# Performance work log

Measured on AMD Instinct MI355X. Metric: run time of the kernel, lower is better.

Reference implementation:

```python
import jax, jax.numpy as jnp
import numpy as np

PSI = 0.001  # convex-combination reconditioning strength
C, N, B = 4, 64, 2048


def _symmap(A, f, psi):
    # recondition via convex combination with identity, then apply f to the spectrum
    if psi > 0:
        A = (1.0 - psi) * A + psi * jnp.eye(A.shape[-1], dtype=A.dtype)
    L, Q = jnp.linalg.eigh(A)
    # Q diag(f(L)) Q^T
    return jnp.einsum('...ik,...k,...jk->...ij', Q, f(L), Q)


def setup_inputs() -> dict:
    key = jax.random.key(0)
    k1, k2 = jax.random.split(key)
    A = jax.random.normal(k1, (B, N, N), dtype=jnp.float32)
    inp = A @ A.swapaxes(-1, -2) / N + 0.1 * jnp.eye(N, dtype=jnp.float32)  # SPD [B,N,N]
    W = jax.random.normal(k2, (C, N, N), dtype=jnp.float32)
    weight = W @ W.swapaxes(-1, -2)  # module init: weight = W W^T, [C,N,N]
    return {'input': inp, 'weight': weight}


def reference(input, weight):
    # Omega^{-1/2} for each of the C tangency points
    ref_sri = _symmap(weight, lambda x: 1.0 / jnp.sqrt(x), PSI)  # [C,N,N]
    # congruence: Omega^{-1/2} Theta Omega^{-1/2}, broadcast over channels -> [B,C,N,N]
    cong = ref_sri @ input[..., None, :, :] @ ref_sri
    cong = 0.5 * (cong + cong.swapaxes(-1, -2))  # resymmetrize for eigh
    # matrix logarithm -> tangent-space vector field [B,C,N,N]
    return _symmap(cong, jnp.log, PSI)
```

## Files before the change

### kernel.cpp

```cpp
#include <hip/hip_runtime.h>
#include <math.h>

#define N 64
#define CSTR 68

typedef float f32x2 __attribute__((ext_vector_type(2)));

struct __align__(16) Smem {
    float mat[N * CSTR];
    float nbuf[2 * N];
    f32x2 obuf[2][N];
};

__device__ __forceinline__ float bperm(int byteaddr, float v) {
    return __int_as_float(__builtin_amdgcn_ds_bpermute(byteaddr, __float_as_int(v)));
}
__device__ __forceinline__ float rlane(float v, int k) {
    return __int_as_float(__builtin_amdgcn_readlane(__float_as_int(v), k));
}
__device__ __forceinline__ float dot4(float4 a, float4 b) {
    return fmaf(a.x, b.x, fmaf(a.y, b.y, fmaf(a.z, b.z, a.w * b.w)));
}

__device__ float jacobi_b128(float4 (&g)[8], int lane, int wid, Smem& S, int max_sweeps) {
    float4* ownc = (float4*)&S.mat[lane * CSTR + 32 * wid];
    float d = 0.f;
#pragma clang loop unroll(disable)
    for (int s = 0; s < max_sweeps; ++s) {
        float nh = 0.f;
#pragma unroll
        for (int i = 0; i < 8; ++i) nh += dot4(g[i], g[i]);
        S.nbuf[wid * N + lane] = nh;
        __syncthreads();
        d = S.nbuf[lane] + S.nbuf[N + lane];
        int anybad = 0, anybig = 0;
#pragma clang loop unroll(disable)
        for (int m = 1; m < N; ++m) {
            const float4* pc = (const float4*)&S.mat[(lane ^ m) * CSTR + 32 * wid];
            float4 t[8];
#pragma unroll
            for (int i = 0; i < 8; ++i) t[i] = pc[i];
            float op = 0.f;
#pragma unroll
            for (int i = 0; i < 8; ++i) op += dot4(g[i], t[i]);
            float doth = bperm((lane ^ m) << 2, d);
            int p = m & 1;
            ((float*)&S.obuf[p][lane])[wid] = op;
            __syncthreads();
            f32x2 ov = S.obuf[p][lane];
            float o = ov.x + ov.y;
            bool is_lo = lane < (lane ^ m);
            float dp = is_lo ? d : doth;
            float dq = is_lo ? doth : d;
            float oo = o * o, pq = dp * dq;
            int roundbad = __any(oo > 4e-10f * pq);
            anybad |= roundbad;
            anybig |= __any(oo > 1e-7f * pq);
            if (!roundbad) continue;
            bool skip = oo <= (1e-24f * pq);
            float osafe = skip ? 1.0f : o;
            float theta = (dq - dp) * 0.5f * __builtin_amdgcn_rcpf(osafe);
            float tt = -copysignf(
                __builtin_amdgcn_rcpf(fabsf(theta) + sqrtf(fmaf(theta, theta, 1.0f))),
                theta);
            float cc = rsqrtf(fmaf(tt, tt, 1.0f));
            float sv = tt * cc;
            cc = skip ? 1.0f : cc;
            sv = skip ? 0.0f : sv;
            float c2 = cc * cc, s2 = sv * sv, cso = 2.0f * cc * sv * o;
            d = is_lo ? fmaf(c2, dp, fmaf(s2, dq, cso))
                      : fmaf(s2, dp, fmaf(c2, dq, -cso));
            d = fmaxf(d, 1e-30f);
            float ss = is_lo ? sv : -sv;
#pragma unroll
            for (int i = 0; i < 8; ++i) {
                g[i].x = fmaf(ss, t[i].x, cc * g[i].x);
                g[i].y = fmaf(ss, t[i].y, cc * g[i].y);
                g[i].z = fmaf(ss, t[i].z, cc * g[i].z);
                g[i].w = fmaf(ss, t[i].w, cc * g[i].w);
            }
#pragma unroll
            for (int i = 0; i < 8; ++i) ownc[i] = g[i];
        }
        if (!__any(anybad) || !anybig) break;
    }
    float nh = 0.f;
#pragma unroll
    for (int i = 0; i < 8; ++i) nh += dot4(g[i], g[i]);
    S.nbuf[wid * N + lane] = nh;
    __syncthreads();
    d = S.nbuf[lane] + S.nbuf[N + lane];
    return d;
}

__device__ void recon_store(const float4 (&g)[8], float coef, int lane, int wid,
                            Smem& S, float* __restrict__ outp) {
    int row0 = wid * 32;
    float4 acc[8];
#pragma unroll
    for (int i = 0; i < 8; ++i) acc[i] = (float4){0.f, 0.f, 0.f, 0.f};
#pragma clang loop unroll(disable)
    for (int k = 0; k < N; ++k) {
        float wk = rlane(coef, k) * S.mat[k * CSTR + lane];
#pragma unroll
        for (int i = 0; i < 8; ++i) {
            acc[i].x = fmaf(rlane(g[i].x, k), wk, acc[i].x);
            acc[i].y = fmaf(rlane(g[i].y, k), wk, acc[i].y);
            acc[i].z = fmaf(rlane(g[i].z, k), wk, acc[i].z);
            acc[i].w = fmaf(rlane(g[i].w, k), wk, acc[i].w);
        }
    }
#pragma unroll
    for (int i = 0; i < 8; ++i) {
        outp[(row0 + 4 * i + 0) * N + lane] = acc[i].x;
        outp[(row0 + 4 * i + 1) * N + lane] = acc[i].y;
        outp[(row0 + 4 * i + 2) * N + lane] = acc[i].z;
        outp[(row0 + 4 * i + 3) * N + lane] = acc[i].w;
    }
}

__global__ __launch_bounds__(128, 4) void prep_R(const float* __restrict__ wgt,
                                                 float* __restrict__ Rws) {
    __shared__ Smem S;
    int c = blockIdx.x;
    int tid = threadIdx.x, wid = tid >> 6, lane = tid & 63;
    int row0 = wid * 32;
    const float* W = wgt + (size_t)c * (N * N);
    float4 g[8];
#pragma unroll
    for (int i = 0; i < 8; ++i) {
        float v[4];
#pragma unroll
        for (int q = 0; q < 4; ++q) {
            int rr = row0 + 4 * i + q;
            v[q] = 0.999f * W[rr * N + lane] + (rr == lane ? 0.001f : 0.f);
        }
        g[i] = (float4){v[0], v[1], v[2], v[3]};
    }
    float4* ownc = (float4*)&S.mat[lane * CSTR + row0];
#pragma unroll
    for (int i = 0; i < 8; ++i) ownc[i] = g[i];
    float d = jacobi_b128(g, lane, wid, S, 15);
    float coef = sqrtf(rsqrtf(d)) / d;
    recon_store(g, coef, lane, wid, S, Rws + (size_t)c * (N * N));
}

__global__ __launch_bounds__(128, 4) void tangent_log(const float* __restrict__ inp,
                                                      const float* __restrict__ Rws,
                                                      float* __restrict__ out) {
    __shared__ Smem S;
    int bid = blockIdx.x, b = bid >> 2, c = bid & 3;
    int tid = threadIdx.x, wid = tid >> 6, lane = tid & 63;
    int row0 = wid * 32;
    const float* Th = inp + (size_t)b * (N * N);
    const float* Rc = Rws + (size_t)c * (N * N);

    f32x2 r[32];
#pragma unroll
    for (int k = 0; k < 32; ++k) {
        r[k].x = Rc[(2 * k) * N + lane];
        r[k].y = Rc[(2 * k + 1) * N + lane];
    }
#pragma clang loop unroll(disable)
    for (int i = 0; i < 32; ++i) {
        const float4* __restrict__ row = (const float4*)(Th + (size_t)(row0 + i) * N);
        f32x2 a = {0.f, 0.f}, bacc = {0.f, 0.f};
#pragma unroll
        for (int q = 0; q < 16; q += 2) {
            float4 v0 = row[q], v1 = row[q + 1];
            a    = (f32x2){v0.x, v0.y} * r[2 * q]     + a;
            a    = (f32x2){v0.z, v0.w} * r[2 * q + 1] + a;
            bacc = (f32x2){v1.x, v1.y} * r[2 * q + 2] + bacc;
            bacc = (f32x2){v1.z, v1.w} * r[2 * q + 3] + bacc;
        }
        f32x2 sres = a + bacc;
        S.mat[lane * CSTR + row0 + i] = sres.x + sres.y;
    }
    __syncthreads();
    f32x2 ucol[32];
    {
        const f32x2* myc = (const f32x2*)&S.mat[lane * CSTR];
#pragma unroll
        for (int k = 0; k < 32; ++k) ucol[k] = myc[k];
    }
    __syncthreads();
#pragma clang loop unroll(disable)
    for (int i = 0; i < 32; ++i) {
        const float4* __restrict__ row = (const float4*)(Rc + (size_t)(row0 + i) * N);
        f32x2 a = {0.f, 0.f}, bacc = {0.f, 0.f};
#pragma unroll
        for (int q = 0; q < 16; q += 2) {
            float4 v0 = row[q], v1 = row[q + 1];
            a    = (f32x2){v0.x, v0.y} * ucol[2 * q]     + a;
            a    = (f32x2){v0.z, v0.w} * ucol[2 * q + 1] + a;
            bacc = (f32x2){v1.x, v1.y} * ucol[2 * q + 2] + bacc;
            bacc = (f32x2){v1.z, v1.w} * ucol[2 * q + 3] + bacc;
        }
        f32x2 sres = a + bacc;
        S.mat[lane * CSTR + row0 + i] = sres.x + sres.y;
    }
    __syncthreads();
    float4 g[8];
    {
        float4 own[8];
        const float4* oc = (const float4*)&S.mat[lane * CSTR + row0];
#pragma unroll
        for (int i = 0; i < 8; ++i) own[i] = oc[i];
        float tr[32];
#pragma unroll
        for (int i = 0; i < 32; ++i) tr[i] = S.mat[(row0 + i) * CSTR + lane];
        __syncthreads();
#pragma unroll
        for (int i = 0; i < 8; ++i) {
            float v[4];
#pragma unroll
            for (int q = 0; q < 4; ++q) {
                int rr = row0 + 4 * i + q;
                float ov = (q == 0) ? own[i].x : (q == 1) ? own[i].y : (q == 2) ? own[i].z : own[i].w;
                float sym = 0.5f * (ov + tr[4 * i + q]);
                v[q] = 0.999f * sym + (rr == lane ? 0.001f : 0.f);
            }
            g[i] = (float4){v[0], v[1], v[2], v[3]};
        }
        float4* wc = (float4*)&S.mat[lane * CSTR + row0];
#pragma unroll
        for (int i = 0; i < 8; ++i) wc[i] = g[i];
    }

    float d = jacobi_b128(g, lane, wid, S, 15);
    float coef = 0.5f * logf(d) / d;
    recon_store(g, coef, lane, wid, S, out + (size_t)bid * (N * N));
}

extern "C" void kernel_launch(void* const* d_in, const int* in_sizes, int n_in,
                              void* d_out, int out_size, void* d_ws, size_t ws_size,
                              hipStream_t stream) {
    const float* inp = (const float*)d_in[0];
    const float* wgt = (const float*)d_in[1];
    float* out = (float*)d_out;
    float* Rws = (float*)d_ws;

    int B = in_sizes[0] / (N * N);
    int C = in_sizes[1] / (N * N);

    hipLaunchKernelGGL(prep_R, dim3(C), dim3(128), 0, stream, wgt, Rws);
    hipLaunchKernelGGL(tangent_log, dim3(B * C), dim3(128), 0, stream, inp, Rws, out);
}
```

Baseline: 4.879 ms.

## Assign one matrix per wavefront to eliminate block barriers in Jacobi

Each 64x64 eigensolve now runs on a single wavefront instead of being split across two waves. This removes the __syncthreads and the LDS partial-dot exchange on every one of the 63 pair rotations per sweep. Each lane holds a full column of 64 floats and works with packed f32x2 FMAs. Two independent matrices share a 128-thread block, each with its own LDS tile. The cost is doubled per-lane register use (launch bounds drop to 2 blocks per CU) and half as many lanes working on each matrix.

```diff
diff --git a/kernel.cpp b/kernel.cpp
--- a/kernel.cpp
+++ b/kernel.cpp
@@ -6,49 +6,53 @@
 
 typedef float f32x2 __attribute__((ext_vector_type(2)));
 
-struct __align__(16) Smem {
-    float mat[N * CSTR];
-    float nbuf[2 * N];
-    f32x2 obuf[2][N];
-};
-
 __device__ __forceinline__ float bperm(int byteaddr, float v) {
     return __int_as_float(__builtin_amdgcn_ds_bpermute(byteaddr, __float_as_int(v)));
 }
 __device__ __forceinline__ float rlane(float v, int k) {
     return __int_as_float(__builtin_amdgcn_readlane(__float_as_int(v), k));
 }
-__device__ __forceinline__ float dot4(float4 a, float4 b) {
-    return fmaf(a.x, b.x, fmaf(a.y, b.y, fmaf(a.z, b.z, a.w * b.w)));
-}
-
-__device__ float jacobi_b128(float4 (&g)[8], int lane, int wid, Smem& S, int max_sweeps) {
-    float4* ownc = (float4*)&S.mat[lane * CSTR + 32 * wid];
+__device__ __forceinline__ f32x2 lo2(float4 v) { return (f32x2){v.x, v.y}; }
+__device__ __forceinline__ f32x2 hi2(float4 v) { return (f32x2){v.z, v.w}; }
+__device__ __forceinline__ float4 join4(f32x2 a, f32x2 b) { return (float4){a.x, a.y, b.x, b.y}; }
+__device__ __forceinline__ f32x2 pkfma(f32x2 a, f32x2 b, f32x2 c) {
+    return __builtin_elementwise_fma(a, b, c);
+}
+
+__device__ float jacobi_wave(float4 (&g)[16], int lane, float* __restrict__ mat,
+                             int max_sweeps) {
+    float4* __restrict__ ownc = (float4*)&mat[lane * CSTR];
     float d = 0.f;
 #pragma clang loop unroll(disable)
     for (int s = 0; s < max_sweeps; ++s) {
-        float nh = 0.f;
-#pragma unroll
-        for (int i = 0; i < 8; ++i) nh += dot4(g[i], g[i]);
-        S.nbuf[wid * N + lane] = nh;
-        __syncthreads();
-        d = S.nbuf[lane] + S.nbuf[N + lane];
+        {
+            f32x2 na = {0.f, 0.f}, nb = {0.f, 0.f};
+#pragma unroll
+            for (int i = 0; i < 16; ++i) {
+                na = pkfma(lo2(g[i]), lo2(g[i]), na);
+                nb = pkfma(hi2(g[i]), hi2(g[i]), nb);
+            }
+            f32x2 ns = na + nb;
+            d = ns.x + ns.y;
+        }
         int anybad = 0, anybig = 0;
 #pragma clang loop unroll(disable)
         for (int m = 1; m < N; ++m) {
-            const float4* pc = (const float4*)&S.mat[(lane ^ m) * CSTR + 32 * wid];
-            float4 t[8];
-#pragma unroll
-            for (int i = 0; i < 8; ++i) t[i] = pc[i];
-            float op = 0.f;
-#pragma unroll
-            for (int i = 0; i < 8; ++i) op += dot4(g[i], t[i]);
+            const float4* __restrict__ pc = (const float4*)&mat[(lane ^ m) * CSTR];
+            float4 t[16];
+#pragma unroll
+            for (int i = 0; i < 16; ++i) t[i] = pc[i];
+            f32x2 oa = {0.f, 0.f}, ob = {0.f, 0.f}, oc = {0.f, 0.f}, od = {0.f, 0.f};
+#pragma unroll
+            for (int i = 0; i < 8; ++i) {
+                oa = pkfma(lo2(g[2 * i]),     lo2(t[2 * i]),     oa);
+                ob = pkfma(hi2(g[2 * i]),     hi2(t[2 * i]),     ob);
+                oc = pkfma(lo2(g[2 * i + 1]), lo2(t[2 * i + 1]), oc);
+                od = pkfma(hi2(g[2 * i + 1]), hi2(t[2 * i + 1]), od);
+            }
+            f32x2 os = (oa + ob) + (oc + od);
+            float o = os.x + os.y;
             float doth = bperm((lane ^ m) << 2, d);
-            int p = m & 1;
-            ((float*)&S.obuf[p][lane])[wid] = op;
-            __syncthreads();
-            f32x2 ov = S.obuf[p][lane];
-            float o = ov.x + ov.y;
             bool is_lo = lane < (lane ^ m);
             float dp = is_lo ? d : doth;
             float dq = is_lo ? doth : d;
@@ -72,164 +76,153 @@
                       : fmaf(s2, dp, fmaf(c2, dq, -cso));
             d = fmaxf(d, 1e-30f);
             float ss = is_lo ? sv : -sv;
-#pragma unroll
-            for (int i = 0; i < 8; ++i) {
-                g[i].x = fmaf(ss, t[i].x, cc * g[i].x);
-                g[i].y = fmaf(ss, t[i].y, cc * g[i].y);
-                g[i].z = fmaf(ss, t[i].z, cc * g[i].z);
-                g[i].w = fmaf(ss, t[i].w, cc * g[i].w);
+            f32x2 cc2 = {cc, cc}, ss2 = {ss, ss};
+#pragma unroll
+            for (int i = 0; i < 16; ++i) {
+                f32x2 glo = pkfma(ss2, lo2(t[i]), lo2(g[i]) * cc2);
+                f32x2 ghi = pkfma(ss2, hi2(t[i]), hi2(g[i]) * cc2);
+                g[i] = join4(glo, ghi);
+                ownc[i] = g[i];
             }
-#pragma unroll
-            for (int i = 0; i < 8; ++i) ownc[i] = g[i];
-        }
-        if (!__any(anybad) || !anybig) break;
-    }
-    float nh = 0.f;
-#pragma unroll
-    for (int i = 0; i < 8; ++i) nh += dot4(g[i], g[i]);
-    S.nbuf[wid * N + lane] = nh;
-    __syncthreads();
-    d = S.nbuf[lane] + S.nbuf[N + lane];
-    return d;
-}
-
-__device__ void recon_store(const float4 (&g)[8], float coef, int lane, int wid,
-                            Smem& S, float* __restrict__ outp) {
-    int row0 = wid * 32;
-    float4 acc[8];
-#pragma unroll
-    for (int i = 0; i < 8; ++i) acc[i] = (float4){0.f, 0.f, 0.f, 0.f};
+        }
+        if (!anybad || !anybig) break;
+    }
+    f32x2 na = {0.f, 0.f}, nb = {0.f, 0.f};
+#pragma unroll
+    for (int i = 0; i < 16; ++i) {
+        na = pkfma(lo2(g[i]), lo2(g[i]), na);
+        nb = pkfma(hi2(g[i]), hi2(g[i]), nb);
+    }
+    f32x2 ns = na + nb;
+    return ns.x + ns.y;
+}
+
+__device__ void recon_store(const float4 (&g)[16], float coef, int lane,
+                            const float* __restrict__ mat, float* __restrict__ outp) {
+    f32x2 acc[32];
+#pragma unroll
+    for (int i = 0; i < 32; ++i) acc[i] = (f32x2){0.f, 0.f};
 #pragma clang loop unroll(disable)
     for (int k = 0; k < N; ++k) {
-        float wk = rlane(coef, k) * S.mat[k * CSTR + lane];
-#pragma unroll
-        for (int i = 0; i < 8; ++i) {
-            acc[i].x = fmaf(rlane(g[i].x, k), wk, acc[i].x);
-            acc[i].y = fmaf(rlane(g[i].y, k), wk, acc[i].y);
-            acc[i].z = fmaf(rlane(g[i].z, k), wk, acc[i].z);
-            acc[i].w = fmaf(rlane(g[i].w, k), wk, acc[i].w);
-        }
-    }
-#pragma unroll
-    for (int i = 0; i < 8; ++i) {
-        outp[(row0 + 4 * i + 0) * N + lane] = acc[i].x;
-        outp[(row0 + 4 * i + 1) * N + lane] = acc[i].y;
-        outp[(row0 + 4 * i + 2) * N + lane] = acc[i].z;
-        outp[(row0 + 4 * i + 3) * N + lane] = acc[i].w;
-    }
-}
-
-__global__ __launch_bounds__(128, 4) void prep_R(const float* __restrict__ wgt,
-                                                 float* __restrict__ Rws) {
-    __shared__ Smem S;
-    int c = blockIdx.x;
+        float wk = rlane(coef, k) * mat[k * CSTR + lane];
+        f32x2 wk2 = {wk, wk};
+#pragma unroll
+        for (int i = 0; i < 16; ++i) {
+            f32x2 b0 = {rlane(g[i].x, k), rlane(g[i].y, k)};
+            f32x2 b1 = {rlane(g[i].z, k), rlane(g[i].w, k)};
+            acc[2 * i]     = pkfma(b0, wk2, acc[2 * i]);
+            acc[2 * i + 1] = pkfma(b1, wk2, acc[2 * i + 1]);
+        }
+    }
+#pragma unroll
+    for (int i = 0; i < 32; ++i) {
+        outp[(size_t)(2 * i) * N + lane]     = acc[i].x;
+        outp[(size_t)(2 * i + 1) * N + lane] = acc[i].y;
+    }
+}
+
+__global__ __launch_bounds__(128, 2) void prep_R(const float* __restrict__ wgt,
+                                                 float* __restrict__ Rws, int C) {
+    __shared__ float S[2][N * CSTR];
     int tid = threadIdx.x, wid = tid >> 6, lane = tid & 63;
-    int row0 = wid * 32;
-    const float* W = wgt + (size_t)c * (N * N);
-    float4 g[8];
-#pragma unroll
-    for (int i = 0; i < 8; ++i) {
-        float v[4];
-#pragma unroll
-        for (int q = 0; q < 4; ++q) {
-            int rr = row0 + 4 * i + q;
-            v[q] = 0.999f * W[rr * N + lane] + (rr == lane ? 0.001f : 0.f);
-        }
-        g[i] = (float4){v[0], v[1], v[2], v[3]};
-    }
-    float4* ownc = (float4*)&S.mat[lane * CSTR + row0];
-#pragma unroll
-    for (int i = 0; i < 8; ++i) ownc[i] = g[i];
-    float d = jacobi_b128(g, lane, wid, S, 15);
+    int c = blockIdx.x * 2 + wid;
+    if (c >= C) return;
+    c = __builtin_amdgcn_readfirstlane(c);
+    const float* __restrict__ W = wgt + (size_t)c * (N * N);
+    float* __restrict__ mat = S[wid];
+    float4 g[16];
+#pragma unroll
+    for (int i = 0; i < 16; ++i) {
+        float v0 = 0.999f * W[(4 * i + 0) * N + lane] + ((4 * i + 0) == lane ? 0.001f : 0.f);
+        float v1 = 0.999f * W[(4 * i + 1) * N + lane] + ((4 * i + 1) == lane ? 0.001f : 0.f);
+        float v2 = 0.999f * W[(4 * i + 2) * N + lane] + ((4 * i + 2) == lane ? 0.001f : 0.f);
+        float v3 = 0.999f * W[(4 * i + 3) * N + lane] + ((4 * i + 3) == lane ? 0.001f : 0.f);
+        g[i] = (float4){v0, v1, v2, v3};
+    }
+    float4* __restrict__ ownc = (float4*)&mat[lane * CSTR];
+#pragma unroll
+    for (int i = 0; i < 16; ++i) ownc[i] = g[i];
+    float d = jacobi_wave(g, lane, mat, 15);
     float coef = sqrtf(rsqrtf(d)) / d;
-    recon_store(g, coef, lane, wid, S, Rws + (size_t)c * (N * N));
-}
-
-__global__ __launch_bounds__(128, 4) void tangent_log(const float* __restrict__ inp,
+    recon_store(g, coef, lane, mat, Rws + (size_t)c * (N * N));
+}
+
+__global__ __launch_bounds__(128, 2) void tangent_log(const float* __restrict__ inp,
                                                       const float* __restrict__ Rws,
-                                                      float* __restrict__ out) {
-    __shared__ Smem S;
-    int bid = blockIdx.x, b = bid >> 2, c = bid & 3;
+                                                      float* __restrict__ out, int total) {
+    __shared__ float S[2][N * CSTR];
     int tid = threadIdx.x, wid = tid >> 6, lane = tid & 63;
-    int row0 = wid * 32;
-    const float* Th = inp + (size_t)b * (N * N);
-    const float* Rc = Rws + (size_t)c * (N * N);
+    int midx = blockIdx.x * 2 + wid;
+    if (midx >= total) return;
+    midx = __builtin_amdgcn_readfirstlane(midx);
+    int b = midx >> 2, c = midx & 3;
+    const float* __restrict__ Th = inp + (size_t)b * (N * N);
+    const float* __restrict__ Rc = Rws + (size_t)c * (N * N);
+    float* __restrict__ mat = S[wid];
 
     f32x2 r[32];
 #pragma unroll
-    for (int k = 0; k < 32; ++k) {
-        r[k].x = Rc[(2 * k) * N + lane];
-        r[k].y = Rc[(2 * k + 1) * N + lane];
-    }
+    for (int k = 0; k < 32; ++k)
+        r[k] = (f32x2){Rc[(2 * k) * N + lane], Rc[(2 * k + 1) * N + lane]};
+
+    f32x2 ucol[32];
 #pragma clang loop unroll(disable)
     for (int i = 0; i < 32; ++i) {
-        const float4* __restrict__ row = (const float4*)(Th + (size_t)(row0 + i) * N);
-        f32x2 a = {0.f, 0.f}, bacc = {0.f, 0.f};
-#pragma unroll
-        for (int q = 0; q < 16; q += 2) {
-            float4 v0 = row[q], v1 = row[q + 1];
-            a    = (f32x2){v0.x, v0.y} * r[2 * q]     + a;
-            a    = (f32x2){v0.z, v0.w} * r[2 * q + 1] + a;
-            bacc = (f32x2){v1.x, v1.y} * r[2 * q + 2] + bacc;
-            bacc = (f32x2){v1.z, v1.w} * r[2 * q + 3] + bacc;
-        }
-        f32x2 sres = a + bacc;
-        S.mat[lane * CSTR + row0 + i] = sres.x + sres.y;
-    }
-    __syncthreads();
-    f32x2 ucol[32];
-    {
-        const f32x2* myc = (const f32x2*)&S.mat[lane * CSTR];
-#pragma unroll
-        for (int k = 0; k < 32; ++k) ucol[k] = myc[k];
-    }
-    __syncthreads();
+        const float4* __restrict__ r0 = (const float4*)(Th + (size_t)(2 * i) * N);
+        const float4* __restrict__ r1 = (const float4*)(Th + (size_t)(2 * i + 1) * N);
+        f32x2 a0 = {0.f, 0.f}, b0 = {0.f, 0.f}, a1 = {0.f, 0.f}, b1 = {0.f, 0.f};
+#pragma unroll
+        for (int q = 0; q < 16; ++q) {
+            float4 v0 = r0[q], v1 = r1[q];
+            a0 = pkfma(lo2(v0), r[2 * q], a0);
+            b0 = pkfma(hi2(v0), r[2 * q + 1], b0);
+            a1 = pkfma(lo2(v1), r[2 * q], a1);
+            b1 = pkfma(hi2(v1), r[2 * q + 1], b1);
+        }
+        f32x2 s0 = a0 + b0, s1 = a1 + b1;
+        ucol[i] = (f32x2){s0.x + s0.y, s1.x + s1.y};
+    }
+    f32x2 mcol[32];
 #pragma clang loop unroll(disable)
     for (int i = 0; i < 32; ++i) {
-        const float4* __restrict__ row = (const float4*)(Rc + (size_t)(row0 + i) * N);
-        f32x2 a = {0.f, 0.f}, bacc = {0.f, 0.f};
-#pragma unroll
-        for (int q = 0; q < 16; q += 2) {
-            float4 v0 = row[q], v1 = row[q + 1];
-            a    = (f32x2){v0.x, v0.y} * ucol[2 * q]     + a;
-            a    = (f32x2){v0.z, v0.w} * ucol[2 * q + 1] + a;
-            bacc = (f32x2){v1.x, v1.y} * ucol[2 * q + 2] + bacc;
-            bacc = (f32x2){v1.z, v1.w} * ucol[2 * q + 3] + bacc;
-        }
-        f32x2 sres = a + bacc;
-        S.mat[lane * CSTR + row0 + i] = sres.x + sres.y;
-    }
-    __syncthreads();
-    float4 g[8];
-    {
-        float4 own[8];
-        const float4* oc = (const float4*)&S.mat[lane * CSTR + row0];
-#pragma unroll
-        for (int i = 0; i < 8; ++i) own[i] = oc[i];
-        float tr[32];
-#pragma unroll
-        for (int i = 0; i < 32; ++i) tr[i] = S.mat[(row0 + i) * CSTR + lane];
-        __syncthreads();
-#pragma unroll
-        for (int i = 0; i < 8; ++i) {
-            float v[4];
-#pragma unroll
-            for (int q = 0; q < 4; ++q) {
-                int rr = row0 + 4 * i + q;
-                float ov = (q == 0) ? own[i].x : (q == 1) ? own[i].y : (q == 2) ? own[i].z : own[i].w;
-                float sym = 0.5f * (ov + tr[4 * i + q]);
-                v[q] = 0.999f * sym + (rr == lane ? 0.001f : 0.f);
-            }
-            g[i] = (float4){v[0], v[1], v[2], v[3]};
-        }
-        float4* wc = (float4*)&S.mat[lane * CSTR + row0];
-#pragma unroll
-        for (int i = 0; i < 8; ++i) wc[i] = g[i];
-    }
-
-    float d = jacobi_b128(g, lane, wid, S, 15);
+        const float4* __restrict__ r0 = (const float4*)(Rc + (size_t)(2 * i) * N);
+        const float4* __restrict__ r1 = (const float4*)(Rc + (size_t)(2 * i + 1) * N);
+        f32x2 a0 = {0.f, 0.f}, b0 = {0.f, 0.f}, a1 = {0.f, 0.f}, b1 = {0.f, 0.f};
+#pragma unroll
+        for (int q = 0; q < 16; ++q) {
+            float4 v0 = r0[q], v1 = r1[q];
+            a0 = pkfma(lo2(v0), ucol[2 * q], a0);
+            b0 = pkfma(hi2(v0), ucol[2 * q + 1], b0);
+            a1 = pkfma(lo2(v1), ucol[2 * q], a1);
+            b1 = pkfma(hi2(v1), ucol[2 * q + 1], b1);
+        }
+        f32x2 s0 = a0 + b0, s1 = a1 + b1;
+        mcol[i] = (f32x2){s0.x + s0.y, s1.x + s1.y};
+    }
+    float4* __restrict__ ownc = (float4*)&mat[lane * CSTR];
+#pragma unroll
+    for (int i = 0; i < 16; ++i) ownc[i] = join4(mcol[2 * i], mcol[2 * i + 1]);
+    float4 g[16];
+#pragma unroll
+    for (int i = 0; i < 16; ++i) {
+        float t0 = mat[(4 * i + 0) * CSTR + lane];
+        float t1 = mat[(4 * i + 1) * CSTR + lane];
+        float t2 = mat[(4 * i + 2) * CSTR + lane];
+        float t3 = mat[(4 * i + 3) * CSTR + lane];
+        f32x2 mlo = mcol[2 * i], mhi = mcol[2 * i + 1];
+        float4 vv;
+        vv.x = 0.999f * (0.5f * (mlo.x + t0)) + ((4 * i + 0) == lane ? 0.001f : 0.f);
+        vv.y = 0.999f * (0.5f * (mlo.y + t1)) + ((4 * i + 1) == lane ? 0.001f : 0.f);
+        vv.z = 0.999f * (0.5f * (mhi.x + t2)) + ((4 * i + 2) == lane ? 0.001f : 0.f);
+        vv.w = 0.999f * (0.5f * (mhi.y + t3)) + ((4 * i + 3) == lane ? 0.001f : 0.f);
+        g[i] = vv;
+    }
+#pragma unroll
+    for (int i = 0; i < 16; ++i) ownc[i] = g[i];
+
+    float d = jacobi_wave(g, lane, mat, 15);
     float coef = 0.5f * logf(d) / d;
-    recon_store(g, coef, lane, wid, S, out + (size_t)bid * (N * N));
+    recon_store(g, coef, lane, mat, out + (size_t)midx * (N * N));
 }
 
 extern "C" void kernel_launch(void* const* d_in, const int* in_sizes, int n_in,
@@ -243,6 +236,7 @@
     int B = in_sizes[0] / (N * N);
     int C = in_sizes[1] / (N * N);
 
-    hipLaunchKernelGGL(prep_R, dim3(C), dim3(128), 0, stream, wgt, Rws);
-    hipLaunchKernelGGL(tangent_log, dim3(B * C), dim3(128), 0, stream, inp, Rws, out);
-}
+    hipLaunchKernelGGL(prep_R, dim3((C + 1) / 2), dim3(128), 0, stream, wgt, Rws, C);
+    hipLaunchKernelGGL(tangent_log, dim3((B * C + 1) / 2), dim3(128), 0, stream,
+                       inp, Rws, out, B * C);
+}
```

After: 4.650 ms. -4.7%, faster.
